# Kernel tuning notes

Hardware: AMD Instinct MI355X
Metric: run time of the kernel (lower is better)

## Reference

```python
import jax, jax.numpy as jnp
import numpy as np

B, MSTEP, NFEAT, ATT = 8192, 200, 64, 64

def setup_inputs() -> dict:
    key = jax.random.key(0)
    k1, k2, k3, k4, k5, k6 = jax.random.split(key, 6)
    sc_q = (6.0 / (NFEAT + ATT)) ** 0.5
    sc_s = (6.0 / (ATT + 1)) ** 0.5
    return {
        "x": jax.random.normal(k1, (B, NFEAT), dtype=jnp.float32),
        "mem": jax.random.normal(k2, (B, MSTEP, NFEAT), dtype=jnp.float32),
        "Wq": jax.random.uniform(k3, (NFEAT, ATT), jnp.float32, -sc_q, sc_q),
        "Wk": jax.random.uniform(k4, (NFEAT, ATT), jnp.float32, -sc_q, sc_q),
        "bias": jax.random.uniform(k5, (ATT,), jnp.float32, -sc_q, sc_q),
        "Ws": jax.random.uniform(k6, (ATT, 1), jnp.float32, -sc_s, sc_s),
    }

def reference(x, mem, Wq, Wk, bias, Ws):
    # query: [B, 1, att]
    query = (x @ Wq)[:, None, :]
    # key: [B, mstep, att]
    key = jnp.einsum("bmf,fa->bma", mem, Wk)
    # additive attention: tanh(q + k + b), scalar score, softmax over mstep
    proj = jnp.tanh(query + key + bias)
    scores = jnp.einsum("bma,ao->bm", proj, Ws)          # [B, mstep]
    weights = jax.nn.softmax(scores, axis=1)              # softmax over mstep
    # context: weighted sum of keys -> [B, att]
    context = jnp.einsum("bm,bma->ba", weights, key)
    return context
```

## Files before the change

kernel.cpp:

```cpp
#include <hip/hip_runtime.h>
#include <math.h>

#define MSTEP 200
#define NF 64
#define NA 64
#define NG 56
#define MPADR 224

__device__ __forceinline__ int memT_off(int f, int g) {
    int slot = (g & ~7) | ((g ^ f) & 7);
    return f * (NG * 4) + slot * 4;
}

__device__ __forceinline__ float ftanh(float x) {
    float e = __expf(2.0f * x);
    return 1.0f - 2.0f / (e + 1.0f);
}

__launch_bounds__(256, 2)
__global__ void customAttention_48515950576474_kernel(
    const float* __restrict__ x, const float* __restrict__ mem,
    const float* __restrict__ Wq, const float* __restrict__ Wk,
    const float* __restrict__ bias, const float* __restrict__ Ws,
    float* __restrict__ out)
{
    __shared__ float memT[NF * NG * 4];
    __shared__ float scores_part[4][MPADR];
    __shared__ float weights[MPADR];
    __shared__ float x_lds[NF];
    __shared__ float ws_lds[NA];
    __shared__ float q_lds[NA];
    __shared__ float wmem_part[4][NF];
    __shared__ float redmax[4], redsum[4];

    const int t    = threadIdx.x;
    const int b    = blockIdx.x;
    const int f    = t & 63;
    const int tg   = t >> 6;
    const int lane = t & 63;
    const int a0   = tg * 16;

    const float* memb = mem + (size_t)b * (MSTEP * NF);

    if (t < NF) {
        x_lds[t]  = x[(size_t)b * NF + t];
        ws_lds[t] = Ws[t];
    }

    #pragma unroll
    for (int p = 0; p < 14; ++p) {
        int g  = tg + 4 * p;
        int m0 = 4 * g;
        float4 v;
        v.x = (m0 + 0 < MSTEP) ? memb[(m0 + 0) * NF + f] : 0.0f;
        v.y = (m0 + 1 < MSTEP) ? memb[(m0 + 1) * NF + f] : 0.0f;
        v.z = (m0 + 2 < MSTEP) ? memb[(m0 + 2) * NF + f] : 0.0f;
        v.w = (m0 + 3 < MSTEP) ? memb[(m0 + 3) * NF + f] : 0.0f;
        *(float4*)&memT[memT_off(f, g)] = v;
    }
    __syncthreads();

    {
        int aj = lane & 15;
        int fh = lane >> 4;
        float qp = 0.0f;
        #pragma unroll
        for (int k = 0; k < 16; ++k) {
            int ff = fh * 16 + k;
            qp += x_lds[ff] * Wq[ff * NA + a0 + aj];
        }
        qp += __shfl_xor(qp, 16);
        qp += __shfl_xor(qp, 32);
        if (fh == 0) q_lds[a0 + aj] = qp + bias[a0 + aj];
    }

    const int g2 = (lane < NG) ? lane : (NG - 1);
    float acc[4][16];
    #pragma unroll
    for (int r = 0; r < 4; ++r)
        #pragma unroll
        for (int j = 0; j < 16; ++j) acc[r][j] = 0.0f;

    const int a0u = __builtin_amdgcn_readfirstlane(a0);

    #pragma unroll 8
    for (int ff = 0; ff < NF; ++ff) {
        float4 mv = *(const float4*)&memT[memT_off(ff, g2)];
        float wkv[16];
        #pragma unroll
        for (int j = 0; j < 16; ++j) wkv[j] = Wk[ff * NA + a0u + j];
        #pragma unroll
        for (int r = 0; r < 4; ++r) {
            float m_r = (r == 0) ? mv.x : (r == 1) ? mv.y : (r == 2) ? mv.z : mv.w;
            #pragma unroll
            for (int j = 0; j < 16; ++j)
                acc[r][j] = fmaf(m_r, wkv[j], acc[r][j]);
        }
    }

    {
        float qv[16], wsv[16];
        #pragma unroll
        for (int j = 0; j < 16; j += 4) {
            *(float4*)&qv[j]  = *(const float4*)&q_lds[a0 + j];
            *(float4*)&wsv[j] = *(const float4*)&ws_lds[a0 + j];
        }
        float sc[4];
        #pragma unroll
        for (int r = 0; r < 4; ++r) {
            float s = 0.0f;
            #pragma unroll
            for (int j = 0; j < 16; ++j)
                s += ftanh(qv[j] + acc[r][j]) * wsv[j];
            sc[r] = s;
        }
        if (lane < NG)
            *(float4*)&scores_part[tg][4 * lane] = make_float4(sc[0], sc[1], sc[2], sc[3]);
    }
    __syncthreads();

    {
        float s = -INFINITY;
        if (t < MPADR) {
            s = scores_part[0][t] + scores_part[1][t] + scores_part[2][t] + scores_part[3][t];
            if (t >= MSTEP) s = -INFINITY;
        }
        float mx = s;
        #pragma unroll
        for (int d = 1; d < 64; d <<= 1) mx = fmaxf(mx, __shfl_xor(mx, d));
        if (lane == 0) redmax[tg] = mx;
        __syncthreads();
        mx = fmaxf(fmaxf(redmax[0], redmax[1]), fmaxf(redmax[2], redmax[3]));
        float e = (t < MSTEP) ? __expf(s - mx) : 0.0f;
        float sm = e;
        #pragma unroll
        for (int d = 1; d < 64; d <<= 1) sm += __shfl_xor(sm, d);
        if (lane == 0) redsum[tg] = sm;
        __syncthreads();
        float tot = redsum[0] + redsum[1] + redsum[2] + redsum[3];
        if (t < MPADR) weights[t] = e / tot;
    }
    __syncthreads();

    {
        float part = 0.0f;
        #pragma unroll
        for (int k = 0; k < 14; ++k) {
            int g = tg * 14 + k;
            float4 mv = *(const float4*)&memT[memT_off(f, g)];
            float4 wv = *(const float4*)&weights[4 * g];
            part = fmaf(mv.x, wv.x, part);
            part = fmaf(mv.y, wv.y, part);
            part = fmaf(mv.z, wv.z, part);
            part = fmaf(mv.w, wv.w, part);
        }
        wmem_part[tg][f] = part;
    }
    __syncthreads();

    {
        float wm = wmem_part[0][lane] + wmem_part[1][lane]
                 + wmem_part[2][lane] + wmem_part[3][lane];
        int aj = lane & 15;
        int fh = lane >> 4;
        float ctx = 0.0f;
        #pragma unroll
        for (int k = 0; k < 16; ++k) {
            int ff = fh * 16 + k;
            float wmf = __shfl(wm, ff);
            ctx = fmaf(wmf, Wk[ff * NA + a0 + aj], ctx);
        }
        ctx += __shfl_xor(ctx, 16);
        ctx += __shfl_xor(ctx, 32);
        if (fh == 0) out[(size_t)b * NA + a0 + aj] = ctx;
    }
}

extern "C" void kernel_launch(void* const* d_in, const int* in_sizes, int n_in,
                              void* d_out, int out_size, void* d_ws, size_t ws_size,
                              hipStream_t stream) {
    const float* x    = (const float*)d_in[0];
    const float* mem  = (const float*)d_in[1];
    const float* Wq   = (const float*)d_in[2];
    const float* Wk   = (const float*)d_in[3];
    const float* bias = (const float*)d_in[4];
    const float* Ws   = (const float*)d_in[5];
    float* out = (float*)d_out;
    const int B = in_sizes[0] / NF;
    customAttention_48515950576474_kernel<<<B, 256, 0, stream>>>(x, mem, Wq, Wk, bias, Ws, out);
}
```

Before: 713.6 us.

## Compute key projection with split-bf16 MFMA and reuse keys for context

The mem@Wk key projection moves from scalar FP32 FMAs to MFMA 16x16x32 bf16 instructions. Both operands are split into high and low bf16 parts, with three products per tile to keep close to FP32 accuracy. The keys stay in registers and are combined directly with the softmax weights for the context, instead of reducing weighted mem and then multiplying by Wk. Loads become vectorised float4 reads into swizzled LDS tiles, which adds bf16 conversion work and per-block Wk staging, plus some precision risk from the split-bf16 approximation.

```diff
diff --git a/kernel.cpp b/kernel.cpp
--- a/kernel.cpp
+++ b/kernel.cpp
@@ -4,18 +4,13 @@
 #define MSTEP 200
 #define NF 64
 #define NA 64
-#define NG 56
-#define MPADR 224
-
-__device__ __forceinline__ int memT_off(int f, int g) {
-    int slot = (g & ~7) | ((g ^ f) & 7);
-    return f * (NG * 4) + slot * 4;
-}
-
-__device__ __forceinline__ float ftanh(float x) {
-    float e = __expf(2.0f * x);
-    return 1.0f - 2.0f / (e + 1.0f);
-}
+#define MROWS 208
+#define NMT 13
+
+typedef __bf16 bf16x4 __attribute__((ext_vector_type(4)));
+typedef __bf16 bf16x8 __attribute__((ext_vector_type(8)));
+typedef float  floatx4 __attribute__((ext_vector_type(4)));
+
 
 __launch_bounds__(256, 2)
 __global__ void customAttention_48515950576474_kernel(
@@ -24,156 +19,205 @@
     const float* __restrict__ bias, const float* __restrict__ Ws,
     float* __restrict__ out)
 {
-    __shared__ float memT[NF * NG * 4];
-    __shared__ float scores_part[4][MPADR];
-    __shared__ float weights[MPADR];
-    __shared__ float x_lds[NF];
-    __shared__ float ws_lds[NA];
+    __shared__ __align__(16) __bf16 mh[MROWS * NF];
+    __shared__ __align__(16) __bf16 ml[MROWS * NF];
+    __shared__ __align__(16) __bf16 wh[NA * NF];
+    __shared__ __align__(16) __bf16 wl[NA * NF];
     __shared__ float q_lds[NA];
-    __shared__ float wmem_part[4][NF];
+    __shared__ float scores[MROWS];
+    __shared__ float weights[MROWS];
+    __shared__ float ctxp[4][NA];
     __shared__ float redmax[4], redsum[4];
 
     const int t    = threadIdx.x;
     const int b    = blockIdx.x;
-    const int f    = t & 63;
-    const int tg   = t >> 6;
+    const int w    = t >> 6;
     const int lane = t & 63;
-    const int a0   = tg * 16;
-
-    const float* memb = mem + (size_t)b * (MSTEP * NF);
-
-    if (t < NF) {
-        x_lds[t]  = x[(size_t)b * NF + t];
-        ws_lds[t] = Ws[t];
-    }
-
-    #pragma unroll
-    for (int p = 0; p < 14; ++p) {
-        int g  = tg + 4 * p;
-        int m0 = 4 * g;
-        float4 v;
-        v.x = (m0 + 0 < MSTEP) ? memb[(m0 + 0) * NF + f] : 0.0f;
-        v.y = (m0 + 1 < MSTEP) ? memb[(m0 + 1) * NF + f] : 0.0f;
-        v.z = (m0 + 2 < MSTEP) ? memb[(m0 + 2) * NF + f] : 0.0f;
-        v.w = (m0 + 3 < MSTEP) ? memb[(m0 + 3) * NF + f] : 0.0f;
-        *(float4*)&memT[memT_off(f, g)] = v;
-    }
-    __syncthreads();
-
-    {
-        int aj = lane & 15;
-        int fh = lane >> 4;
-        float qp = 0.0f;
-        #pragma unroll
-        for (int k = 0; k < 16; ++k) {
-            int ff = fh * 16 + k;
-            qp += x_lds[ff] * Wq[ff * NA + a0 + aj];
+
+    const float4* memb4 = (const float4*)(mem + (size_t)b * (MSTEP * NF));
+    for (int it = 0; it < 13; ++it) {
+        int fi = t + (it << 8);
+        if (fi < MSTEP * 16) {
+            float4 v = memb4[fi];
+            int m = fi >> 4, qq = fi & 15;
+            int eo = m * 64 + (((qq >> 1) ^ (m & 7)) << 3) + ((qq & 1) << 2);
+            float vv[4] = {v.x, v.y, v.z, v.w};
+            bf16x4 h, l;
+            #pragma unroll
+            for (int j = 0; j < 4; ++j) {
+                __bf16 hb = (__bf16)vv[j];
+                h[j] = hb;
+                l[j] = (__bf16)(vv[j] - (float)hb);
+            }
+            *(bf16x4*)&mh[eo] = h;
+            *(bf16x4*)&ml[eo] = l;
+        }
+    }
+    if (t < 64) {
+        int m = MSTEP + (t >> 3), c = t & 7;
+        int eo = m * 64 + ((c ^ (m & 7)) << 3);
+        *(float4*)&mh[eo] = make_float4(0.f, 0.f, 0.f, 0.f);
+        *(float4*)&ml[eo] = make_float4(0.f, 0.f, 0.f, 0.f);
+    }
+
+    for (int i = 0; i < 16; ++i) {
+        int idx = t + (i << 8);
+        int kk = idx >> 6, a = idx & 63;
+        float v = Wk[idx];
+        __bf16 hb = (__bf16)v;
+        int eo = a * 64 + ((((kk >> 3) ^ (a & 7))) << 3) + (kk & 7);
+        wh[eo] = hb;
+        wl[eo] = (__bf16)(v - (float)hb);
+    }
+
+    {
+        float xv = x[(size_t)b * NF + lane];
+        int aj = lane & 15, fh = lane >> 4;
+        int a0 = w << 4;
+        float qp = 0.f;
+        #pragma unroll
+        for (int kx = 0; kx < 16; ++kx) {
+            int ff = fh * 16 + kx;
+            qp = fmaf(__shfl(xv, ff), Wq[ff * NA + a0 + aj], qp);
         }
         qp += __shfl_xor(qp, 16);
         qp += __shfl_xor(qp, 32);
         if (fh == 0) q_lds[a0 + aj] = qp + bias[a0 + aj];
     }
-
-    const int g2 = (lane < NG) ? lane : (NG - 1);
-    float acc[4][16];
+    __syncthreads();
+
+    bf16x8 bh[4][2], bl[4][2];
+    {
+        int a = lane & 15, ko = lane >> 4;
+        #pragma unroll
+        for (int at = 0; at < 4; ++at) {
+            int row = at * 16 + a;
+            #pragma unroll
+            for (int kc = 0; kc < 2; ++kc) {
+                int eo = row * 64 + (((kc * 4 + ko) ^ (row & 7)) << 3);
+                bh[at][kc] = *(const bf16x8*)&wh[eo];
+                bl[at][kc] = *(const bf16x8*)&wl[eo];
+            }
+        }
+    }
+
+    floatx4 kreg[4][4];
     #pragma unroll
-    for (int r = 0; r < 4; ++r)
-        #pragma unroll
-        for (int j = 0; j < 16; ++j) acc[r][j] = 0.0f;
-
-    const int a0u = __builtin_amdgcn_readfirstlane(a0);
-
-    #pragma unroll 8
-    for (int ff = 0; ff < NF; ++ff) {
-        float4 mv = *(const float4*)&memT[memT_off(ff, g2)];
-        float wkv[16];
-        #pragma unroll
-        for (int j = 0; j < 16; ++j) wkv[j] = Wk[ff * NA + a0u + j];
-        #pragma unroll
-        for (int r = 0; r < 4; ++r) {
-            float m_r = (r == 0) ? mv.x : (r == 1) ? mv.y : (r == 2) ? mv.z : mv.w;
-            #pragma unroll
-            for (int j = 0; j < 16; ++j)
-                acc[r][j] = fmaf(m_r, wkv[j], acc[r][j]);
-        }
-    }
-
-    {
-        float qv[16], wsv[16];
-        #pragma unroll
-        for (int j = 0; j < 16; j += 4) {
-            *(float4*)&qv[j]  = *(const float4*)&q_lds[a0 + j];
-            *(float4*)&wsv[j] = *(const float4*)&ws_lds[a0 + j];
-        }
-        float sc[4];
-        #pragma unroll
-        for (int r = 0; r < 4; ++r) {
-            float s = 0.0f;
-            #pragma unroll
-            for (int j = 0; j < 16; ++j)
-                s += ftanh(qv[j] + acc[r][j]) * wsv[j];
-            sc[r] = s;
-        }
-        if (lane < NG)
-            *(float4*)&scores_part[tg][4 * lane] = make_float4(sc[0], sc[1], sc[2], sc[3]);
-    }
-    __syncthreads();
-
-    {
-        float s = -INFINITY;
-        if (t < MPADR) {
-            s = scores_part[0][t] + scores_part[1][t] + scores_part[2][t] + scores_part[3][t];
-            if (t >= MSTEP) s = -INFINITY;
-        }
-        float mx = s;
+    for (int i = 0; i < 4; ++i)
+        #pragma unroll
+        for (int at = 0; at < 4; ++at)
+            kreg[i][at] = (floatx4){0.f, 0.f, 0.f, 0.f};
+
+    float qv[4], wsv[4];
+    #pragma unroll
+    for (int at = 0; at < 4; ++at) {
+        int a = at * 16 + (lane & 15);
+        qv[at]  = q_lds[a];
+        wsv[at] = Ws[a];
+    }
+
+    #pragma unroll
+    for (int i = 0; i < 4; ++i) {
+        int mt = w + 4 * i;
+        if (mt < NMT) {
+            int m = mt * 16 + (lane & 15);
+            int ko = lane >> 4;
+            bf16x8 ah[2], al[2];
+            #pragma unroll
+            for (int kc = 0; kc < 2; ++kc) {
+                int eo = m * 64 + (((kc * 4 + ko) ^ (m & 7)) << 3);
+                ah[kc] = *(const bf16x8*)&mh[eo];
+                al[kc] = *(const bf16x8*)&ml[eo];
+            }
+            #pragma unroll
+            for (int at = 0; at < 4; ++at) {
+                floatx4 acc = kreg[i][at];
+                #pragma unroll
+                for (int kc = 0; kc < 2; ++kc) {
+                    acc = __builtin_amdgcn_mfma_f32_16x16x32_bf16(ah[kc], bh[at][kc], acc, 0, 0, 0);
+                    acc = __builtin_amdgcn_mfma_f32_16x16x32_bf16(ah[kc], bl[at][kc], acc, 0, 0, 0);
+                    acc = __builtin_amdgcn_mfma_f32_16x16x32_bf16(al[kc], bh[at][kc], acc, 0, 0, 0);
+                }
+                kreg[i][at] = acc;
+            }
+            float s[4] = {0.f, 0.f, 0.f, 0.f};
+            #pragma unroll
+            for (int at = 0; at < 4; ++at) {
+                #pragma unroll
+                for (int r = 0; r < 4; ++r) {
+                    float e  = __expf(2.f * (kreg[i][at][r] + qv[at]));
+                    float th = 1.f - 2.f / (e + 1.f);
+                    s[r] = fmaf(th, wsv[at], s[r]);
+                }
+            }
+            #pragma unroll
+            for (int r = 0; r < 4; ++r) {
+                s[r] += __shfl_xor(s[r], 1);
+                s[r] += __shfl_xor(s[r], 2);
+                s[r] += __shfl_xor(s[r], 4);
+                s[r] += __shfl_xor(s[r], 8);
+            }
+            if ((lane & 15) == 0) {
+                int mrow = mt * 16 + (lane >> 4) * 4;
+                scores[mrow + 0] = s[0];
+                scores[mrow + 1] = s[1];
+                scores[mrow + 2] = s[2];
+                scores[mrow + 3] = s[3];
+            }
+        }
+    }
+    __syncthreads();
+
+    {
+        float sv = (t < MSTEP) ? scores[t] : -INFINITY;
+        float mx = sv;
         #pragma unroll
         for (int d = 1; d < 64; d <<= 1) mx = fmaxf(mx, __shfl_xor(mx, d));
-        if (lane == 0) redmax[tg] = mx;
+        if (lane == 0) redmax[w] = mx;
         __syncthreads();
         mx = fmaxf(fmaxf(redmax[0], redmax[1]), fmaxf(redmax[2], redmax[3]));
-        float e = (t < MSTEP) ? __expf(s - mx) : 0.0f;
+        float e = (t < MSTEP) ? __expf(sv - mx) : 0.f;
         float sm = e;
         #pragma unroll
         for (int d = 1; d < 64; d <<= 1) sm += __shfl_xor(sm, d);
-        if (lane == 0) redsum[tg] = sm;
+        if (lane == 0) redsum[w] = sm;
         __syncthreads();
         float tot = redsum[0] + redsum[1] + redsum[2] + redsum[3];
-        if (t < MPADR) weights[t] = e / tot;
-    }
-    __syncthreads();
-
-    {
-        float part = 0.0f;
-        #pragma unroll
-        for (int k = 0; k < 14; ++k) {
-            int g = tg * 14 + k;
-            float4 mv = *(const float4*)&memT[memT_off(f, g)];
-            float4 wv = *(const float4*)&weights[4 * g];
-            part = fmaf(mv.x, wv.x, part);
-            part = fmaf(mv.y, wv.y, part);
-            part = fmaf(mv.z, wv.z, part);
-            part = fmaf(mv.w, wv.w, part);
-        }
-        wmem_part[tg][f] = part;
-    }
-    __syncthreads();
-
-    {
-        float wm = wmem_part[0][lane] + wmem_part[1][lane]
-                 + wmem_part[2][lane] + wmem_part[3][lane];
-        int aj = lane & 15;
-        int fh = lane >> 4;
-        float ctx = 0.0f;
-        #pragma unroll
-        for (int k = 0; k < 16; ++k) {
-            int ff = fh * 16 + k;
-            float wmf = __shfl(wm, ff);
-            ctx = fmaf(wmf, Wk[ff * NA + a0 + aj], ctx);
-        }
-        ctx += __shfl_xor(ctx, 16);
-        ctx += __shfl_xor(ctx, 32);
-        if (fh == 0) out[(size_t)b * NA + a0 + aj] = ctx;
-    }
+        if (t < MROWS) weights[t] = e / tot;
+    }
+    __syncthreads();
+
+    {
+        float c[4] = {0.f, 0.f, 0.f, 0.f};
+        #pragma unroll
+        for (int i = 0; i < 4; ++i) {
+            int mt = w + 4 * i;
+            if (mt < NMT) {
+                int mrow = mt * 16 + (lane >> 4) * 4;
+                #pragma unroll
+                for (int r = 0; r < 4; ++r) {
+                    float wv = weights[mrow + r];
+                    #pragma unroll
+                    for (int at = 0; at < 4; ++at)
+                        c[at] = fmaf(wv, kreg[i][at][r], c[at]);
+                }
+            }
+        }
+        #pragma unroll
+        for (int at = 0; at < 4; ++at) {
+            c[at] += __shfl_xor(c[at], 16);
+            c[at] += __shfl_xor(c[at], 32);
+        }
+        if (lane < 16) {
+            #pragma unroll
+            for (int at = 0; at < 4; ++at)
+                ctxp[w][at * 16 + lane] = c[at];
+        }
+    }
+    __syncthreads();
+
+    if (t < NA)
+        out[(size_t)b * NA + t] = ctxp[0][t] + ctxp[1][t] + ctxp[2][t] + ctxp[3][t];
 }
 
 extern "C" void kernel_launch(void* const* d_in, const int* in_sizes, int n_in,
```

Measured after the change: 655.5 us. 1.09x faster.
